# Kernel optimization log

Measured on AMD Instinct MI355X. Metric: run time of the kernel, lower is better.

Reference implementation:

```python
import jax, jax.numpy as jnp
import numpy as np

N = 100000
F_IN = 128
DIM = 2
E = 3200000


def setup_inputs() -> dict:
    key = jax.random.key(0)
    k1, k2, k3, k4, k5, k6, k7 = jax.random.split(key, 7)
    x = jax.random.normal(k1, (N, F_IN), dtype=jnp.float32)
    edge_index = jax.random.randint(k2, (2, E), 0, N, dtype=jnp.int64)
    edge_attr = jax.random.uniform(k3, (E,), dtype=jnp.float32)
    # GCNConv params: lin weight [F_IN, DIM] (glorot), bias zeros
    conv_w = jax.random.normal(k4, (F_IN, DIM), dtype=jnp.float32) * (1.0 / np.sqrt(F_IN))
    conv_b = jnp.zeros((DIM,), dtype=jnp.float32)
    # TopKPooling score weight [DIM]
    pool_w = jax.random.normal(k5, (DIM,), dtype=jnp.float32)
    # fc: Linear(N*DIM, 1), init normal(0, 0.01), bias 0 (per init_weights)
    fc_w = jax.random.normal(k6, (N * DIM, 1), dtype=jnp.float32) * 0.01
    fc_b = jnp.zeros((1,), dtype=jnp.float32)
    return {"x": x, "edge_index": edge_index, "edge_attr": edge_attr,
            "conv_w": conv_w, "conv_b": conv_b, "pool_w": pool_w,
            "fc_w": fc_w, "fc_b": fc_b}


def reference(x, edge_index, edge_attr, conv_w, conv_b, pool_w, fc_w, fc_b):
    n = x.shape[0]
    row, col = edge_index[0], edge_index[1]
    # --- GCNConv: add self-loops (weight 1), symmetric normalization ---
    loop = jnp.arange(n, dtype=edge_index.dtype)
    row_f = jnp.concatenate([row, loop])
    col_f = jnp.concatenate([col, loop])
    w_f = jnp.concatenate([edge_attr, jnp.ones((n,), dtype=x.dtype)])
    deg = jax.ops.segment_sum(w_f, col_f, num_segments=n)  # [N]
    dinv = jnp.where(deg > 0, jax.lax.rsqrt(deg), 0.0)
    norm = dinv[row_f] * w_f * dinv[col_f]  # [E+N]
    h = x @ conv_w  # [N, DIM] transform-then-propagate
    msg = norm[:, None] * h[row_f]  # [E+N, DIM]
    out = jax.ops.segment_sum(msg, col_f, num_segments=n) + conv_b  # [N, DIM]
    # --- ReLU ---
    out = jax.nn.relu(out)
    # --- TopKPooling with k = N (single graph): score, sort desc, gate ---
    score = jnp.tanh((out @ pool_w) / jnp.linalg.norm(pool_w))  # [N]
    perm = jnp.argsort(-score)
    pooled = out[perm] * score[perm][:, None]  # [N, DIM]
    # --- flatten + fc + sigmoid ---
    flat = pooled.reshape(-1)  # [N*DIM]
    y = jax.nn.sigmoid(flat @ fc_w + fc_b)  # [1]
    return y
```

## Files before the change

### kernel.cpp

```cpp
#include <hip/hip_runtime.h>
#include <math.h>

#define FIN 128
#define W 512
#define S 16
#define MAXG 256
#define CAP 18432u
#define HB 256
#define HT 1024
#define BP 200

__device__ __forceinline__ long long edge_at(const void* p, long long i, unsigned mode) {
  return mode ? ((const long long*)p)[i] : (long long)((const int*)p)[i];
}

__device__ __forceinline__ void atomic_fadd(float* p, float v) {
  __hip_atomic_fetch_add(p, v, __ATOMIC_RELAXED, __HIP_MEMORY_SCOPE_AGENT);
}

__global__ void k_detect(const unsigned* ei, unsigned* mode, float* acc,
                         unsigned* cur, int G, unsigned* ticket) {
  int t = threadIdx.x;
  if (t == 0) {
    unsigned orv = 0;
    for (int i = 1; i < 1024; i += 2) orv |= ei[i];
    *mode = (orv == 0) ? 1u : 0u;
    *acc = 0.0f;
    *ticket = 0u;
  }
  for (int i = t; i < G; i += 64) cur[i] = (unsigned)i * CAP;
}

__global__ void k_h(const float* __restrict__ x, const float* __restrict__ cw,
                    float* __restrict__ h, int n) {
  int gt = blockIdx.x * blockDim.x + threadIdx.x;
  int node = gt >> 5;
  int sub = gt & 31;
  if (node >= n) return;
  float4 xv = ((const float4*)x)[node * 32 + sub];
  float s0 = xv.x * cw[sub * 8 + 0] + xv.y * cw[sub * 8 + 2] +
             xv.z * cw[sub * 8 + 4] + xv.w * cw[sub * 8 + 6];
  float s1 = xv.x * cw[sub * 8 + 1] + xv.y * cw[sub * 8 + 3] +
             xv.z * cw[sub * 8 + 5] + xv.w * cw[sub * 8 + 7];
  for (int off = 16; off > 0; off >>= 1) {
    s0 += __shfl_down(s0, off, 32);
    s1 += __shfl_down(s1, off, 32);
  }
  if (sub == 0) { h[node * 2] = s0; h[node * 2 + 1] = s1; }
}

__global__ void k_scatter2(const void* ei, const float* __restrict__ attr,
                           long long E, int G, unsigned* cur,
                           uint2* __restrict__ packed,
                           const unsigned* __restrict__ mode) {
  __shared__ unsigned hist[MAXG];
  __shared__ unsigned base[MAXG];
  unsigned m = *mode;
  int t = threadIdx.x;
  if (t < MAXG) hist[t] = 0;
  __syncthreads();
  long long perB = (E + HB - 1) / HB;
  long long b0 = (long long)blockIdx.x * perB;
  long long lim = b0 + perB; if (lim > E) lim = E;
  long long e = b0 + t;
  for (; e + 3LL * HT < lim; e += 4LL * HT) {
    int c0 = (int)edge_at(ei, E + e, m);
    int c1 = (int)edge_at(ei, E + e + HT, m);
    int c2 = (int)edge_at(ei, E + e + 2 * HT, m);
    int c3 = (int)edge_at(ei, E + e + 3 * HT, m);
    atomicAdd(&hist[c0 >> 9], 1u);
    atomicAdd(&hist[c1 >> 9], 1u);
    atomicAdd(&hist[c2 >> 9], 1u);
    atomicAdd(&hist[c3 >> 9], 1u);
  }
  for (; e < lim; e += HT) {
    int c = (int)edge_at(ei, E + e, m);
    atomicAdd(&hist[c >> 9], 1u);
  }
  __syncthreads();
  if (t < G) base[t] = atomicAdd(&cur[t], hist[t]);
  __syncthreads();
  e = b0 + t;
  for (; e + 3LL * HT < lim; e += 4LL * HT) {
    int r0 = (int)edge_at(ei, e, m),          c0 = (int)edge_at(ei, E + e, m);
    int r1 = (int)edge_at(ei, e + HT, m),     c1 = (int)edge_at(ei, E + e + HT, m);
    int r2 = (int)edge_at(ei, e + 2 * HT, m), c2 = (int)edge_at(ei, E + e + 2 * HT, m);
    int r3 = (int)edge_at(ei, e + 3 * HT, m), c3 = (int)edge_at(ei, E + e + 3 * HT, m);
    float a0 = attr[e], a1 = attr[e + HT], a2 = attr[e + 2 * HT], a3 = attr[e + 3 * HT];
    unsigned p0 = atomicAdd(&base[c0 >> 9], 1u);
    packed[p0] = make_uint2(((unsigned)r0 << 9) | ((unsigned)c0 & 511u), __float_as_uint(a0));
    unsigned p1 = atomicAdd(&base[c1 >> 9], 1u);
    packed[p1] = make_uint2(((unsigned)r1 << 9) | ((unsigned)c1 & 511u), __float_as_uint(a1));
    unsigned p2 = atomicAdd(&base[c2 >> 9], 1u);
    packed[p2] = make_uint2(((unsigned)r2 << 9) | ((unsigned)c2 & 511u), __float_as_uint(a2));
    unsigned p3 = atomicAdd(&base[c3 >> 9], 1u);
    packed[p3] = make_uint2(((unsigned)r3 << 9) | ((unsigned)c3 & 511u), __float_as_uint(a3));
  }
  for (; e < lim; e += HT) {
    int r = (int)edge_at(ei, e, m);
    int c = (int)edge_at(ei, E + e, m);
    float a = attr[e];
    unsigned pos = atomicAdd(&base[c >> 9], 1u);
    packed[pos] = make_uint2(((unsigned)r << 9) | ((unsigned)c & 511u), __float_as_uint(a));
  }
}

__global__ void k_deginv(const uint2* __restrict__ packed, const unsigned* __restrict__ cur,
                         const float* __restrict__ h, float* __restrict__ dinv,
                         float* __restrict__ gv, int n) {
  __shared__ float sdeg[W];
  int g = blockIdx.x, t = threadIdx.x;
  sdeg[t] = 0.f;
  __syncthreads();
  unsigned lo = (unsigned)g * CAP, hi = cur[g];
  for (unsigned b = lo + t; b < hi; b += 4 * 512) {
    unsigned k1 = b + 512, k2 = b + 1024, k3 = b + 1536;
    uint2 p0 = packed[b];
    uint2 p1 = packed[k1 < hi ? k1 : b];
    uint2 p2 = packed[k2 < hi ? k2 : b];
    uint2 p3 = packed[k3 < hi ? k3 : b];
    atomicAdd(&sdeg[p0.x & (W - 1u)], __uint_as_float(p0.y));
    if (k1 < hi) atomicAdd(&sdeg[p1.x & (W - 1u)], __uint_as_float(p1.y));
    if (k2 < hi) atomicAdd(&sdeg[p2.x & (W - 1u)], __uint_as_float(p2.y));
    if (k3 < hi) atomicAdd(&sdeg[p3.x & (W - 1u)], __uint_as_float(p3.y));
  }
  __syncthreads();
  int c = g * W + t;
  if (c < n) {
    float di = rsqrtf(1.0f + sdeg[t]);
    dinv[c] = di;
    gv[2 * c]     = di * h[2 * c];
    gv[2 * c + 1] = di * h[2 * c + 1];
  }
}

__global__ void k_pmsg(const uint2* __restrict__ packed, const unsigned* __restrict__ cur,
                       const float* __restrict__ gv, float* __restrict__ pacc) {
  __shared__ float sacc[2 * W];
  int blk = blockIdx.x, t = threadIdx.x;
  int g = blk >> 4, s = blk & (S - 1);
#pragma unroll
  for (int i = 0; i < 4; ++i) sacc[t + 256 * i] = 0.f;
  __syncthreads();
  unsigned lo = (unsigned)g * CAP, hi = cur[g];
  unsigned len = hi - lo;
  unsigned per = (len + S - 1) / S;
  unsigned mylo = lo + s * per;
  unsigned myhi = mylo + per; if (myhi > hi) myhi = hi;
  const float2* g2 = (const float2*)gv;
  for (unsigned b = mylo + t; b < myhi; b += 4 * 256) {
    unsigned k1 = b + 256, k2 = b + 512, k3 = b + 768;
    uint2 p0 = packed[b];
    uint2 p1 = packed[k1 < myhi ? k1 : b];
    uint2 p2 = packed[k2 < myhi ? k2 : b];
    uint2 p3 = packed[k3 < myhi ? k3 : b];
    float2 g0 = g2[p0.x >> 9];
    float2 g1 = g2[p1.x >> 9];
    float2 g2v = g2[p2.x >> 9];
    float2 g3 = g2[p3.x >> 9];
    float a0 = __uint_as_float(p0.y), a1 = __uint_as_float(p1.y);
    float a2 = __uint_as_float(p2.y), a3 = __uint_as_float(p3.y);
    unsigned c0 = p0.x & (W - 1u), c1 = p1.x & (W - 1u);
    unsigned c2 = p2.x & (W - 1u), c3 = p3.x & (W - 1u);
    atomicAdd(&sacc[2 * c0],     a0 * g0.x);
    atomicAdd(&sacc[2 * c0 + 1], a0 * g0.y);
    if (k1 < myhi) { atomicAdd(&sacc[2 * c1], a1 * g1.x); atomicAdd(&sacc[2 * c1 + 1], a1 * g1.y); }
    if (k2 < myhi) { atomicAdd(&sacc[2 * c2], a2 * g2v.x); atomicAdd(&sacc[2 * c2 + 1], a2 * g2v.y); }
    if (k3 < myhi) { atomicAdd(&sacc[2 * c3], a3 * g3.x); atomicAdd(&sacc[2 * c3 + 1], a3 * g3.y); }
  }
  __syncthreads();
#pragma unroll
  for (int i = 0; i < 4; ++i) pacc[(size_t)blk * (2 * W) + t + 256 * i] = sacc[t + 256 * i];
}

__global__ void k_gout(const float* __restrict__ pacc, const float* __restrict__ dinv,
                       const float* __restrict__ h, const float* __restrict__ cb,
                       const float* __restrict__ pw, float* __restrict__ out,
                       float* __restrict__ score, unsigned* __restrict__ keys,
                       unsigned* __restrict__ table, int n) {
  __shared__ unsigned hist[256];
  int g = blockIdx.x, t = threadIdx.x;
  if (t < 256) hist[t] = 0;
  __syncthreads();
  const float2* p2 = (const float2*)pacc;
  float a0 = 0.f, a1 = 0.f;
#pragma unroll
  for (int s = 0; s < S; ++s) {
    float2 v = p2[(size_t)(g * S + s) * W + t];
    a0 += v.x; a1 += v.y;
  }
  int c = g * W + t;
  if (c < n) {
    float dc = dinv[c];
    float o0 = fmaxf(dc * a0 + dc * dc * h[2 * c]     + cb[0], 0.f);
    float o1 = fmaxf(dc * a1 + dc * dc * h[2 * c + 1] + cb[1], 0.f);
    out[2 * c] = o0; out[2 * c + 1] = o1;
    float pw0 = pw[0], pw1 = pw[1];
    float s = tanhf((o0 * pw0 + o1 * pw1) / sqrtf(pw0 * pw0 + pw1 * pw1));
    score[c] = s;
    unsigned u = __float_as_uint(s);
    unsigned asc = u ^ ((u >> 31) ? 0xFFFFFFFFu : 0x80000000u);
    unsigned key = ~asc;
    keys[c] = key;
    atomicAdd(&hist[key & 255u], 1u);
  }
  __syncthreads();
  if (t < 256) table[t * BP + g] = hist[t];
}

__global__ void k_rhist(const unsigned* __restrict__ keys, int n, int shift,
                        unsigned* table) {
  __shared__ unsigned hist[256];
  int t = threadIdx.x;
  if (t < 256) hist[t] = 0;
  __syncthreads();
  int g = blockIdx.x * 512 + t;
  if (g < n) atomicAdd(&hist[(keys[g] >> shift) & 255u], 1u);
  __syncthreads();
  if (t < 256) table[t * BP + blockIdx.x] = hist[t];
}

__global__ void k_rscat(const unsigned* __restrict__ keysIn,
                        const unsigned* __restrict__ payIn, int n, int shift,
                        const unsigned* __restrict__ table,
                        unsigned* keysOut, unsigned* payOut, int flags) {
  __shared__ unsigned pfx[256];
  __shared__ unsigned scn[256];
  __shared__ unsigned waveCnt[8 * 256];
  int b = blockIdx.x, t = threadIdx.x;
  int lane = t & 63, w = t >> 6;
  int nblk = gridDim.x;
  unsigned rt_total = 0;
  if (t < 256) {
    const unsigned* row = table + t * BP;
    unsigned partial = 0, total = 0;
#pragma unroll 4
    for (int i = 0; i < nblk; ++i) {
      unsigned v = row[i];
      total += v;
      partial += (i < b) ? v : 0u;
    }
    rt_total = total;
    scn[t] = total;
    pfx[t] = partial;
  }
  __syncthreads();
  for (int off = 1; off < 256; off <<= 1) {
    unsigned add = 0;
    if (t < 256 && t >= off) add = scn[t - off];
    __syncthreads();
    if (t < 256) scn[t] += add;
    __syncthreads();
  }
  if (t < 256) pfx[t] += scn[t] - rt_total;
  for (int q = t; q < 8 * 256; q += 512) waveCnt[q] = 0;
  __syncthreads();
  int g = b * 512 + t;
  bool active = g < n;
  unsigned key = 0, pay = 0, d = 0;
  if (active) {
    key = keysIn[g];
    pay = (flags & 1) ? (unsigned)g : payIn[g];
    d = (key >> shift) & 255u;
  }
  unsigned long long am = __ballot(active);
  unsigned long long mm = ~0ull;
#pragma unroll
  for (int bb = 0; bb < 8; ++bb) {
    unsigned long long bl = __ballot((d >> bb) & 1u);
    mm &= ((d >> bb) & 1u) ? bl : ~bl;
  }
  mm &= am;
  int rankw = __popcll(mm & ((1ull << lane) - 1ull));
  if (active && rankw == 0) waveCnt[w * 256 + d] = (unsigned)__popcll(mm);
  __syncthreads();
  if (active) {
    unsigned o = (unsigned)rankw;
    for (int ww = 0; ww < w; ++ww) o += waveCnt[ww * 256 + d];
    unsigned gpos = pfx[d] + o;
    if (!(flags & 2)) keysOut[gpos] = key;
    payOut[gpos] = pay;
  }
}

__global__ void k_final(const unsigned* __restrict__ perm, const float* __restrict__ out,
                        const float* __restrict__ score, const float* __restrict__ fcw,
                        const float* __restrict__ fcb, float* acc, unsigned* ticket,
                        float* y, int n) {
  __shared__ float red[4];
  int stride = gridDim.x * blockDim.x;
  float s = 0.f;
  const float2* o2 = (const float2*)out;
  const float2* f2 = (const float2*)fcw;
  for (int j = blockIdx.x * blockDim.x + threadIdx.x; j < n; j += stride) {
    unsigned p = perm[j];
    float2 ov = o2[p];
    float2 fv = f2[j];
    s += score[p] * (ov.x * fv.x + ov.y * fv.y);
  }
  int lane = threadIdx.x & 63, w = threadIdx.x >> 6;
  for (int off = 32; off > 0; off >>= 1) s += __shfl_down(s, off);
  if (lane == 0) red[w] = s;
  __syncthreads();
  if (threadIdx.x == 0) {
    float bs = red[0] + red[1] + red[2] + red[3];
    atomic_fadd(acc, bs);
    __threadfence();
    unsigned old = __hip_atomic_fetch_add(ticket, 1u, __ATOMIC_ACQ_REL,
                                          __HIP_MEMORY_SCOPE_AGENT);
    if (old == (unsigned)(gridDim.x - 1)) {
      float z = __hip_atomic_fetch_add(acc, 0.0f, __ATOMIC_ACQUIRE,
                                       __HIP_MEMORY_SCOPE_AGENT);
      y[0] = 1.f / (1.f + expf(-(z + fcb[0])));
    }
  }
}

extern "C" void kernel_launch(void* const* d_in, const int* in_sizes, int n_in,
                              void* d_out, int out_size, void* d_ws, size_t ws_size,
                              hipStream_t stream) {
  const float* x     = (const float*)d_in[0];
  const void*  ei    = d_in[1];
  const float* attr  = (const float*)d_in[2];
  const float* convw = (const float*)d_in[3];
  const float* convb = (const float*)d_in[4];
  const float* poolw = (const float*)d_in[5];
  const float* fcw   = (const float*)d_in[6];
  const float* fcb   = (const float*)d_in[7];
  float* y = (float*)d_out;

  int N = in_sizes[0] / FIN;
  long long E = in_sizes[2];
  int G = (N + W - 1) / W;

  float* ws = (float*)d_ws;
  size_t off = 0;
  uint2* packed  = (uint2*)(ws + off); off += (size_t)2 * G * CAP;
  float* pacc    = ws + off; off += (size_t)2 * G * S * W;
  float* h       = ws + off; off += (size_t)2 * N;
  float* dinv    = ws + off; off += (size_t)N;
  float* gv      = ws + off; off += (size_t)2 * N;
  float* outN    = ws + off; off += (size_t)2 * N;
  float* score   = ws + off; off += (size_t)N;
  unsigned* keysA = (unsigned*)(ws + off); off += (size_t)N;
  unsigned* payA  = (unsigned*)(ws + off); off += (size_t)N;
  unsigned* keysB = (unsigned*)(ws + off); off += (size_t)N;
  unsigned* payB  = (unsigned*)(ws + off); off += (size_t)N;
  unsigned* cur   = (unsigned*)(ws + off); off += (size_t)G;
  unsigned* stab  = (unsigned*)(ws + off); off += (size_t)256 * BP;
  float* acc      = ws + off; off += 1;
  unsigned* mode  = (unsigned*)(ws + off); off += 1;
  unsigned* ticket = (unsigned*)(ws + off); off += 1;

  k_detect<<<1, 64, 0, stream>>>((const unsigned*)ei, mode, acc, cur, G, ticket);
  k_h<<<(N * 32 + 255) / 256, 256, 0, stream>>>(x, convw, h, N);

  k_scatter2<<<HB, HT, 0, stream>>>(ei, attr, E, G, cur, packed, mode);

  k_deginv<<<G, W, 0, stream>>>(packed, cur, h, dinv, gv, N);
  k_pmsg<<<G * S, 256, 0, stream>>>(packed, cur, gv, pacc);
  k_gout<<<G, W, 0, stream>>>(pacc, dinv, h, convb, poolw, outN, score, keysA, stab, N);

  k_rscat<<<G, 512, 0, stream>>>(keysA, payB, N, 0, stab, keysB, payB, 1);
  k_rhist<<<G, 512, 0, stream>>>(keysB, N, 8, stab);
  k_rscat<<<G, 512, 0, stream>>>(keysB, payB, N, 8, stab, keysA, payA, 0);
  k_rhist<<<G, 512, 0, stream>>>(keysA, N, 16, stab);
  k_rscat<<<G, 512, 0, stream>>>(keysA, payA, N, 16, stab, keysB, payB, 0);
  k_rhist<<<G, 512, 0, stream>>>(keysB, N, 24, stab);
  k_rscat<<<G, 512, 0, stream>>>(keysB, payB, N, 24, stab, keysA, payA, 2);

  k_final<<<G, 256, 0, stream>>>(payA, outN, score, fcw, fcb, acc, ticket, y, N);
}
```

Baseline: 199.9 us.

## Vectorize edge loads and pad buckets for fixed-trip deginv/pmsg loops

```diff
diff --git a/kernel.cpp b/kernel.cpp
--- a/kernel.cpp
+++ b/kernel.cpp
@@ -3,16 +3,12 @@
 
 #define FIN 128
 #define W 512
-#define S 16
+#define S 18
 #define MAXG 256
 #define CAP 18432u
-#define HB 256
+#define HB 512
 #define HT 1024
 #define BP 200
-
-__device__ __forceinline__ long long edge_at(const void* p, long long i, unsigned mode) {
-  return mode ? ((const long long*)p)[i] : (long long)((const int*)p)[i];
-}
 
 __device__ __forceinline__ void atomic_fadd(float* p, float v) {
   __hip_atomic_fetch_add(p, v, __ATOMIC_RELAXED, __HIP_MEMORY_SCOPE_AGENT);
@@ -59,70 +55,83 @@
   int t = threadIdx.x;
   if (t < MAXG) hist[t] = 0;
   __syncthreads();
-  long long perB = (E + HB - 1) / HB;
+  long long perB = (((E + HB - 1) / HB) + 1) & ~1LL;
   long long b0 = (long long)blockIdx.x * perB;
   long long lim = b0 + perB; if (lim > E) lim = E;
-  long long e = b0 + t;
-  for (; e + 3LL * HT < lim; e += 4LL * HT) {
-    int c0 = (int)edge_at(ei, E + e, m);
-    int c1 = (int)edge_at(ei, E + e + HT, m);
-    int c2 = (int)edge_at(ei, E + e + 2 * HT, m);
-    int c3 = (int)edge_at(ei, E + e + 3 * HT, m);
-    atomicAdd(&hist[c0 >> 9], 1u);
-    atomicAdd(&hist[c1 >> 9], 1u);
-    atomicAdd(&hist[c2 >> 9], 1u);
-    atomicAdd(&hist[c3 >> 9], 1u);
-  }
-  for (; e < lim; e += HT) {
-    int c = (int)edge_at(ei, E + e, m);
-    atomicAdd(&hist[c >> 9], 1u);
+  if (m) {
+    const int4* cc = (const int4*)((const long long*)ei + E);
+    for (long long e = b0 + 2 * t; e < lim; e += 2LL * HT) {
+      int4 v = cc[e >> 1];
+      atomicAdd(&hist[(unsigned)v.x >> 9], 1u);
+      if (e + 1 < lim) atomicAdd(&hist[(unsigned)v.z >> 9], 1u);
+    }
+  } else {
+    const int2* cc = (const int2*)((const int*)ei + E);
+    for (long long e = b0 + 2 * t; e < lim; e += 2LL * HT) {
+      int2 v = cc[e >> 1];
+      atomicAdd(&hist[(unsigned)v.x >> 9], 1u);
+      if (e + 1 < lim) atomicAdd(&hist[(unsigned)v.y >> 9], 1u);
+    }
   }
   __syncthreads();
   if (t < G) base[t] = atomicAdd(&cur[t], hist[t]);
   __syncthreads();
-  e = b0 + t;
-  for (; e + 3LL * HT < lim; e += 4LL * HT) {
-    int r0 = (int)edge_at(ei, e, m),          c0 = (int)edge_at(ei, E + e, m);
-    int r1 = (int)edge_at(ei, e + HT, m),     c1 = (int)edge_at(ei, E + e + HT, m);
-    int r2 = (int)edge_at(ei, e + 2 * HT, m), c2 = (int)edge_at(ei, E + e + 2 * HT, m);
-    int r3 = (int)edge_at(ei, e + 3 * HT, m), c3 = (int)edge_at(ei, E + e + 3 * HT, m);
-    float a0 = attr[e], a1 = attr[e + HT], a2 = attr[e + 2 * HT], a3 = attr[e + 3 * HT];
-    unsigned p0 = atomicAdd(&base[c0 >> 9], 1u);
-    packed[p0] = make_uint2(((unsigned)r0 << 9) | ((unsigned)c0 & 511u), __float_as_uint(a0));
-    unsigned p1 = atomicAdd(&base[c1 >> 9], 1u);
-    packed[p1] = make_uint2(((unsigned)r1 << 9) | ((unsigned)c1 & 511u), __float_as_uint(a1));
-    unsigned p2 = atomicAdd(&base[c2 >> 9], 1u);
-    packed[p2] = make_uint2(((unsigned)r2 << 9) | ((unsigned)c2 & 511u), __float_as_uint(a2));
-    unsigned p3 = atomicAdd(&base[c3 >> 9], 1u);
-    packed[p3] = make_uint2(((unsigned)r3 << 9) | ((unsigned)c3 & 511u), __float_as_uint(a3));
-  }
-  for (; e < lim; e += HT) {
-    int r = (int)edge_at(ei, e, m);
-    int c = (int)edge_at(ei, E + e, m);
-    float a = attr[e];
-    unsigned pos = atomicAdd(&base[c >> 9], 1u);
-    packed[pos] = make_uint2(((unsigned)r << 9) | ((unsigned)c & 511u), __float_as_uint(a));
-  }
-}
-
-__global__ void k_deginv(const uint2* __restrict__ packed, const unsigned* __restrict__ cur,
+  if (m) {
+    const int4* rr = (const int4*)ei;
+    const int4* cc = (const int4*)((const long long*)ei + E);
+    const float2* aa = (const float2*)attr;
+    for (long long e = b0 + 2 * t; e < lim; e += 2LL * HT) {
+      int4 vr = rr[e >> 1];
+      int4 vc = cc[e >> 1];
+      float2 av = aa[e >> 1];
+      unsigned p0 = atomicAdd(&base[(unsigned)vc.x >> 9], 1u);
+      packed[p0] = make_uint2(((unsigned)vr.x << 9) | ((unsigned)vc.x & 511u),
+                              __float_as_uint(av.x));
+      if (e + 1 < lim) {
+        unsigned p1 = atomicAdd(&base[(unsigned)vc.z >> 9], 1u);
+        packed[p1] = make_uint2(((unsigned)vr.z << 9) | ((unsigned)vc.z & 511u),
+                                __float_as_uint(av.y));
+      }
+    }
+  } else {
+    const int2* rr = (const int2*)ei;
+    const int2* cc = (const int2*)((const int*)ei + E);
+    const float2* aa = (const float2*)attr;
+    for (long long e = b0 + 2 * t; e < lim; e += 2LL * HT) {
+      int2 vr = rr[e >> 1];
+      int2 vc = cc[e >> 1];
+      float2 av = aa[e >> 1];
+      unsigned p0 = atomicAdd(&base[(unsigned)vc.x >> 9], 1u);
+      packed[p0] = make_uint2(((unsigned)vr.x << 9) | ((unsigned)vc.x & 511u),
+                              __float_as_uint(av.x));
+      if (e + 1 < lim) {
+        unsigned p1 = atomicAdd(&base[(unsigned)vc.y >> 9], 1u);
+        packed[p1] = make_uint2(((unsigned)vr.y << 9) | ((unsigned)vc.y & 511u),
+                                __float_as_uint(av.y));
+      }
+    }
+  }
+}
+
+__global__ void k_fill(const unsigned* __restrict__ cur, uint2* __restrict__ packed) {
+  int g = blockIdx.x, t = threadIdx.x;
+  unsigned hi = cur[g], end = (unsigned)(g + 1) * CAP;
+  for (unsigned i = hi + t; i < end; i += 256) packed[i] = make_uint2(0u, 0u);
+}
+
+__global__ void k_deginv(const uint2* __restrict__ packed,
                          const float* __restrict__ h, float* __restrict__ dinv,
                          float* __restrict__ gv, int n) {
   __shared__ float sdeg[W];
   int g = blockIdx.x, t = threadIdx.x;
   sdeg[t] = 0.f;
   __syncthreads();
-  unsigned lo = (unsigned)g * CAP, hi = cur[g];
-  for (unsigned b = lo + t; b < hi; b += 4 * 512) {
-    unsigned k1 = b + 512, k2 = b + 1024, k3 = b + 1536;
-    uint2 p0 = packed[b];
-    uint2 p1 = packed[k1 < hi ? k1 : b];
-    uint2 p2 = packed[k2 < hi ? k2 : b];
-    uint2 p3 = packed[k3 < hi ? k3 : b];
-    atomicAdd(&sdeg[p0.x & (W - 1u)], __uint_as_float(p0.y));
-    if (k1 < hi) atomicAdd(&sdeg[p1.x & (W - 1u)], __uint_as_float(p1.y));
-    if (k2 < hi) atomicAdd(&sdeg[p2.x & (W - 1u)], __uint_as_float(p2.y));
-    if (k3 < hi) atomicAdd(&sdeg[p3.x & (W - 1u)], __uint_as_float(p3.y));
+  const uint4* p4 = (const uint4*)(packed + (size_t)g * CAP);
+#pragma unroll 6
+  for (int i = 0; i < (int)((CAP / 2) / 512); ++i) {
+    uint4 v = p4[i * 512 + t];
+    atomicAdd(&sdeg[v.x & (W - 1u)], __uint_as_float(v.y));
+    atomicAdd(&sdeg[v.z & (W - 1u)], __uint_as_float(v.w));
   }
   __syncthreads();
   int c = g * W + t;
@@ -134,43 +143,38 @@
   }
 }
 
-__global__ void k_pmsg(const uint2* __restrict__ packed, const unsigned* __restrict__ cur,
+__global__ void k_pmsg(const uint2* __restrict__ packed,
                        const float* __restrict__ gv, float* __restrict__ pacc) {
   __shared__ float sacc[2 * W];
   int blk = blockIdx.x, t = threadIdx.x;
-  int g = blk >> 4, s = blk & (S - 1);
+  int g = blk / S, s = blk - g * S;
 #pragma unroll
   for (int i = 0; i < 4; ++i) sacc[t + 256 * i] = 0.f;
   __syncthreads();
-  unsigned lo = (unsigned)g * CAP, hi = cur[g];
-  unsigned len = hi - lo;
-  unsigned per = (len + S - 1) / S;
-  unsigned mylo = lo + s * per;
-  unsigned myhi = mylo + per; if (myhi > hi) myhi = hi;
+  const uint4* p4 = (const uint4*)(packed + (size_t)g * CAP + (size_t)s * (CAP / S));
   const float2* g2 = (const float2*)gv;
-  for (unsigned b = mylo + t; b < myhi; b += 4 * 256) {
-    unsigned k1 = b + 256, k2 = b + 512, k3 = b + 768;
-    uint2 p0 = packed[b];
-    uint2 p1 = packed[k1 < myhi ? k1 : b];
-    uint2 p2 = packed[k2 < myhi ? k2 : b];
-    uint2 p3 = packed[k3 < myhi ? k3 : b];
-    float2 g0 = g2[p0.x >> 9];
-    float2 g1 = g2[p1.x >> 9];
-    float2 g2v = g2[p2.x >> 9];
-    float2 g3 = g2[p3.x >> 9];
-    float a0 = __uint_as_float(p0.y), a1 = __uint_as_float(p1.y);
-    float a2 = __uint_as_float(p2.y), a3 = __uint_as_float(p3.y);
-    unsigned c0 = p0.x & (W - 1u), c1 = p1.x & (W - 1u);
-    unsigned c2 = p2.x & (W - 1u), c3 = p3.x & (W - 1u);
-    atomicAdd(&sacc[2 * c0],     a0 * g0.x);
-    atomicAdd(&sacc[2 * c0 + 1], a0 * g0.y);
-    if (k1 < myhi) { atomicAdd(&sacc[2 * c1], a1 * g1.x); atomicAdd(&sacc[2 * c1 + 1], a1 * g1.y); }
-    if (k2 < myhi) { atomicAdd(&sacc[2 * c2], a2 * g2v.x); atomicAdd(&sacc[2 * c2 + 1], a2 * g2v.y); }
-    if (k3 < myhi) { atomicAdd(&sacc[2 * c3], a3 * g3.x); atomicAdd(&sacc[2 * c3 + 1], a3 * g3.y); }
-  }
+  uint4 v0 = p4[t];
+  uint4 v1 = p4[t + 256];
+  float2 ga = g2[v0.x >> 9];
+  float2 gb = g2[v0.z >> 9];
+  float2 gc = g2[v1.x >> 9];
+  float2 gd = g2[v1.z >> 9];
+  float a0 = __uint_as_float(v0.y), a1 = __uint_as_float(v0.w);
+  float a2 = __uint_as_float(v1.y), a3 = __uint_as_float(v1.w);
+  unsigned c0 = v0.x & 511u, c1 = v0.z & 511u;
+  unsigned c2 = v1.x & 511u, c3 = v1.z & 511u;
+  atomicAdd(&sacc[2 * c0],     a0 * ga.x);
+  atomicAdd(&sacc[2 * c0 + 1], a0 * ga.y);
+  atomicAdd(&sacc[2 * c1],     a1 * gb.x);
+  atomicAdd(&sacc[2 * c1 + 1], a1 * gb.y);
+  atomicAdd(&sacc[2 * c2],     a2 * gc.x);
+  atomicAdd(&sacc[2 * c2 + 1], a2 * gc.y);
+  atomicAdd(&sacc[2 * c3],     a3 * gd.x);
+  atomicAdd(&sacc[2 * c3 + 1], a3 * gd.y);
   __syncthreads();
 #pragma unroll
-  for (int i = 0; i < 4; ++i) pacc[(size_t)blk * (2 * W) + t + 256 * i] = sacc[t + 256 * i];
+  for (int i = 0; i < 4; ++i)
+    pacc[(size_t)blk * (2 * W) + t + 256 * i] = sacc[t + 256 * i];
 }
 
 __global__ void k_gout(const float* __restrict__ pacc, const float* __restrict__ dinv,
@@ -356,9 +360,10 @@
   k_h<<<(N * 32 + 255) / 256, 256, 0, stream>>>(x, convw, h, N);
 
   k_scatter2<<<HB, HT, 0, stream>>>(ei, attr, E, G, cur, packed, mode);
-
-  k_deginv<<<G, W, 0, stream>>>(packed, cur, h, dinv, gv, N);
-  k_pmsg<<<G * S, 256, 0, stream>>>(packed, cur, gv, pacc);
+  k_fill<<<G, 256, 0, stream>>>(cur, packed);
+
+  k_deginv<<<G, W, 0, stream>>>(packed, h, dinv, gv, N);
+  k_pmsg<<<G * S, 256, 0, stream>>>(packed, gv, pacc);
   k_gout<<<G, W, 0, stream>>>(pacc, dinv, h, convb, poolw, outN, score, keysA, stab, N);
 
   k_rscat<<<G, 512, 0, stream>>>(keysA, payB, N, 0, stab, keysB, payB, 1);
```

New measurement: 218.9 us. 1.1x slower.
